# Kernel tuning notes

Measured on AMD Instinct MI355X. Metric: run time of the kernel, lower is better.

Reference implementation:

```python
import jax, jax.numpy as jnp
import numpy as np

N_NODES = 100000
N_EDGES = 1600000
C = 64       # in_channels == filters
K = 3        # Chebyshev order
EPS = 1e-5   # InstanceNorm eps


def setup_inputs() -> dict:
    key = jax.random.key(0)
    ks = jax.random.split(key, 8)
    x = jax.random.normal(ks[0], (N_NODES, C), dtype=jnp.float32)
    edge_index = jax.random.randint(ks[1], (2, N_EDGES), 0, N_NODES, dtype=jnp.int64)
    scale = 1.0 / np.sqrt(C)
    W1 = jax.random.normal(ks[2], (K, C, C), dtype=jnp.float32) * scale
    b1 = jnp.zeros((C,), dtype=jnp.float32)
    W2 = jax.random.normal(ks[3], (K, C, C), dtype=jnp.float32) * scale
    b2 = jnp.zeros((C,), dtype=jnp.float32)
    return {"x": x, "edge_index": edge_index, "W1": W1, "b1": b1, "W2": W2, "b2": b2}


def _cheb_conv(x, src, dst, w_edge, W, b, n):
    # PyG ChebConv, norm='sym', lambda_max=2: L_hat = -D^{-1/2} A D^{-1/2}
    def prop(h):  # h: [N, C] -> L_hat @ h via gather -> weight -> scatter-add
        return jax.ops.segment_sum(w_edge[:, None] * h[src], dst, num_segments=n)
    Tx0 = x
    Tx1 = prop(x)
    Tx2 = 2.0 * prop(Tx1) - Tx0
    return Tx0 @ W[0] + Tx1 @ W[1] + Tx2 @ W[2] + b


def _instance_norm(h):
    # PyG InstanceNorm (single graph, affine=False): normalize over nodes per channel
    m = h.mean(axis=0, keepdims=True)
    v = h.var(axis=0, keepdims=True)
    return (h - m) * jax.lax.rsqrt(v + EPS)


def reference(x, edge_index, W1, b1, W2, b2):
    n = x.shape[0]
    src, dst = edge_index[0], edge_index[1]
    ones = jnp.ones((src.shape[0],), dtype=x.dtype)
    deg = jax.ops.segment_sum(ones, dst, num_segments=n)
    safe = jnp.where(deg > 0, deg, 1.0)
    dinv = jnp.where(deg > 0, jax.lax.rsqrt(safe), 0.0)
    w_edge = -dinv[src] * dinv[dst]  # scaled-Laplacian edge weights
    h = _instance_norm(jax.nn.relu(_cheb_conv(x, src, dst, w_edge, W1, b1, n)))
    h = _instance_norm(jax.nn.relu(_cheb_conv(h, src, dst, w_edge, W2, b2, n)))
    return h
```

## Files before the change

kernel.cpp:

```cpp
#include <hip/hip_runtime.h>
#include <hip/hip_fp16.h>

#define NCH 64
#define EPS 1e-5f
#define SBANKS 32
#define BSHIFT 8
#define NBLKA 256
#define SRCMASK 0x1FFFFu
#define QW_SCALE 32767.0f
#define QW_INV (1.0f/32767.0f)

typedef _Float16 f16x8 __attribute__((ext_vector_type(8)));
typedef float f32x4 __attribute__((ext_vector_type(4)));

__global__ __launch_bounds__(256) void k_front(const float* __restrict__ x, __half* __restrict__ xh,
                                               int castTotal, int castB,
                                               const float* __restrict__ W1, _Float16* __restrict__ Wb1,
                                               const float* __restrict__ W2, _Float16* __restrict__ Wb2,
                                               const int* __restrict__ dst, int* __restrict__ cnt,
                                               int E, int per, int nbuck) {
    int bid = blockIdx.x;
    if (bid < castB) {
        int i = (bid * 256 + threadIdx.x) * 4;
        if (i < castTotal) {
            float4 f = *(const float4*)(x + i);
            __half2* o = (__half2*)(xh + i);
            o[0] = __floats2half2_rn(f.x, f.y);
            o[1] = __floats2half2_rn(f.z, f.w);
        }
        return;
    }
    if (bid < castB + 96) {
        int wb = bid - castB;
        const float* W = (wb < 48) ? W1 : W2;
        _Float16* Wb = (wb < 48) ? Wb1 : Wb2;
        int idx = (wb % 48) * 256 + threadIdx.x;
        int j = idx & 7;
        int lane = (idx >> 3) & 63;
        int tk = idx >> 9;
        int tile = tk / 6, kk = tk % 6;
        int k = kk * 32 + (lane >> 4) * 8 + j;
        int n = tile * 16 + (lane & 15);
        Wb[idx] = (_Float16)W[k * 64 + n];
        return;
    }
    __shared__ int lh[512];
    int hb = bid - castB - 96;
    for (int t = threadIdx.x; t < nbuck; t += 256) lh[t] = 0;
    __syncthreads();
    int lo = hb * per, hi = min(E, lo + per);
    for (int e = lo + threadIdx.x; e < hi; e += 256)
        atomicAdd(&lh[dst[e] >> BSHIFT], 1);
    __syncthreads();
    for (int t = threadIdx.x; t < nbuck; t += 256)
        if (lh[t]) atomicAdd(&cnt[t], lh[t]);
}

__global__ void k_bscan(const int* __restrict__ cnt, int* __restrict__ gbase,
                        int* __restrict__ gcur, int nbuck, int E) {
    __shared__ int s[512];
    int t = threadIdx.x;
    int v = (t < nbuck) ? cnt[t] : 0;
    s[t] = v;
    __syncthreads();
    for (int off = 1; off < 512; off <<= 1) {
        int add = (t >= off) ? s[t - off] : 0;
        __syncthreads();
        s[t] += add;
        __syncthreads();
    }
    if (t < nbuck) { int ex = s[t] - v; gbase[t] = ex; gcur[t] = ex; }
    if (t == 0) gbase[nbuck] = E;
}

__global__ __launch_bounds__(256) void k_bin(const int* __restrict__ src,
                                             const int* __restrict__ dst,
                                             int* __restrict__ gcur,
                                             int2* __restrict__ binned, int E, int per, int nbuck) {
    __shared__ int lh[512];
    __shared__ int lcur[512];
    for (int t = threadIdx.x; t < nbuck; t += 256) lh[t] = 0;
    __syncthreads();
    int lo = blockIdx.x * per, hi = min(E, lo + per);
    for (int e = lo + threadIdx.x; e < hi; e += 256)
        atomicAdd(&lh[dst[e] >> BSHIFT], 1);
    __syncthreads();
    for (int t = threadIdx.x; t < nbuck; t += 256) {
        int c = lh[t];
        lcur[t] = c ? atomicAdd(&gcur[t], c) : 0;
    }
    __syncthreads();
    for (int e = lo + threadIdx.x; e < hi; e += 256) {
        int d = dst[e];
        int b = d >> BSHIFT;
        int pos = atomicAdd(&lcur[b], 1);
        binned[pos] = make_int2(src[e], d);
    }
}

__global__ __launch_bounds__(256) void k_bucket(const int2* __restrict__ binned,
                                                const int* __restrict__ gbase,
                                                float* __restrict__ dinv,
                                                int* __restrict__ rowstart,
                                                unsigned int* __restrict__ csr, int N, int nbuck, int E) {
    __shared__ int hist[256];
    __shared__ int lcur[256];
    __shared__ int ltmp[256];
    int b = blockIdx.x;
    int t = threadIdx.x;
    int nodeLo = b << BSHIFT;
    int nHere = min(256, N - nodeLo);
    int e0 = gbase[b], e1 = gbase[b + 1];
    hist[t] = 0;
    __syncthreads();
    for (int e = e0 + t; e < e1; e += 256)
        atomicAdd(&hist[binned[e].y - nodeLo], 1);
    __syncthreads();
    int deg = (t < nHere) ? hist[t] : 0;
    if (t < nHere) dinv[nodeLo + t] = (deg > 0) ? rsqrtf((float)deg) : 0.0f;
    ltmp[t] = deg;
    __syncthreads();
    for (int off = 1; off < 256; off <<= 1) {
        int add = (t >= off) ? ltmp[t - off] : 0;
        __syncthreads();
        ltmp[t] += add;
        __syncthreads();
    }
    int lstart = ltmp[t] - deg;
    if (t < nHere) rowstart[nodeLo + t] = e0 + lstart;
    if (b == nbuck - 1 && t == 0) rowstart[N] = E;
    lcur[t] = lstart;
    __syncthreads();
    for (int e = e0 + t; e < e1; e += 256) {
        int2 sd = binned[e];
        int dl = sd.y - nodeLo;
        int pos = atomicAdd(&lcur[dl], 1);
        unsigned int dd = (unsigned int)min(hist[dl], 32767);
        csr[e0 + pos] = (unsigned int)sd.x | (dd << 17);
    }
}

__global__ void k_weights(unsigned int* __restrict__ csr, const float* __restrict__ dinv, int E) {
    int e = blockIdx.x * blockDim.x + threadIdx.x;
    if (e < E) {
        unsigned int v = csr[e];
        unsigned int s = v & SRCMASK;
        float dd = rsqrtf((float)(v >> 17));
        float aw = dinv[s] * dd;
        unsigned int qw = (unsigned int)(aw * QW_SCALE + 0.5f);
        csr[e] = s | (qw << 17);
    }
}

__global__ __launch_bounds__(256) void k_prop(const __half* __restrict__ h,
                                              const int* __restrict__ rowstart,
                                              const unsigned int* __restrict__ csr,
                                              const __half* __restrict__ tx0,
                                              __half* __restrict__ y, int N,
                                              const float* __restrict__ gstats,
                                              const float* __restrict__ tstats) {
    int lane = threadIdx.x & 63;
    int wv = (blockIdx.x * 256 + threadIdx.x) >> 6;
    int g = lane >> 3, li = lane & 7;
    int node = wv * 8 + g;
    int e = 0, e1 = 0;
    if (node < N) { e = rowstart[node]; e1 = rowstart[node + 1]; }
    float acc[8] = {0.f, 0.f, 0.f, 0.f, 0.f, 0.f, 0.f, 0.f};
    float sw = 0.0f;
    for (; e + 2 <= e1; e += 2) {
        unsigned int v0 = csr[e], v1 = csr[e + 1];
        uint4 a = *(const uint4*)(h + (size_t)(v0 & SRCMASK) * NCH + li * 8);
        uint4 bq = *(const uint4*)(h + (size_t)(v1 & SRCMASK) * NCH + li * 8);
        float w0 = -(float)(v0 >> 17) * QW_INV;
        float w1 = -(float)(v1 >> 17) * QW_INV;
        sw += w0 + w1;
        float2 f;
        f = __half22float2(*(__half2*)&a.x);  acc[0] = fmaf(w0, f.x, acc[0]); acc[1] = fmaf(w0, f.y, acc[1]);
        f = __half22float2(*(__half2*)&a.y);  acc[2] = fmaf(w0, f.x, acc[2]); acc[3] = fmaf(w0, f.y, acc[3]);
        f = __half22float2(*(__half2*)&a.z);  acc[4] = fmaf(w0, f.x, acc[4]); acc[5] = fmaf(w0, f.y, acc[5]);
        f = __half22float2(*(__half2*)&a.w);  acc[6] = fmaf(w0, f.x, acc[6]); acc[7] = fmaf(w0, f.y, acc[7]);
        f = __half22float2(*(__half2*)&bq.x); acc[0] = fmaf(w1, f.x, acc[0]); acc[1] = fmaf(w1, f.y, acc[1]);
        f = __half22float2(*(__half2*)&bq.y); acc[2] = fmaf(w1, f.x, acc[2]); acc[3] = fmaf(w1, f.y, acc[3]);
        f = __half22float2(*(__half2*)&bq.z); acc[4] = fmaf(w1, f.x, acc[4]); acc[5] = fmaf(w1, f.y, acc[5]);
        f = __half22float2(*(__half2*)&bq.w); acc[6] = fmaf(w1, f.x, acc[6]); acc[7] = fmaf(w1, f.y, acc[7]);
    }
    if (e < e1) {
        unsigned int v0 = csr[e];
        uint4 a = *(const uint4*)(h + (size_t)(v0 & SRCMASK) * NCH + li * 8);
        float w0 = -(float)(v0 >> 17) * QW_INV;
        sw += w0;
        float2 f;
        f = __half22float2(*(__half2*)&a.x);  acc[0] = fmaf(w0, f.x, acc[0]); acc[1] = fmaf(w0, f.y, acc[1]);
        f = __half22float2(*(__half2*)&a.y);  acc[2] = fmaf(w0, f.x, acc[2]); acc[3] = fmaf(w0, f.y, acc[3]);
        f = __half22float2(*(__half2*)&a.z);  acc[4] = fmaf(w0, f.x, acc[4]); acc[5] = fmaf(w0, f.y, acc[5]);
        f = __half22float2(*(__half2*)&a.w);  acc[6] = fmaf(w0, f.x, acc[6]); acc[7] = fmaf(w0, f.y, acc[7]);
    }
    if (node >= N) return;
    if (gstats != nullptr) {
        float4 m0 = *(const float4*)(gstats + li * 8);
        float4 m1 = *(const float4*)(gstats + li * 8 + 4);
        float4 r0 = *(const float4*)(gstats + 64 + li * 8);
        float4 r1 = *(const float4*)(gstats + 64 + li * 8 + 4);
        acc[0] = r0.x * (acc[0] - m0.x * sw);
        acc[1] = r0.y * (acc[1] - m0.y * sw);
        acc[2] = r0.z * (acc[2] - m0.z * sw);
        acc[3] = r0.w * (acc[3] - m0.w * sw);
        acc[4] = r1.x * (acc[4] - m1.x * sw);
        acc[5] = r1.y * (acc[5] - m1.y * sw);
        acc[6] = r1.z * (acc[6] - m1.z * sw);
        acc[7] = r1.w * (acc[7] - m1.w * sw);
    }
    if (tx0 != nullptr) {
        uint4 tq = *(const uint4*)(tx0 + (size_t)node * NCH + li * 8);
        float tv[8];
        float2 f;
        f = __half22float2(*(__half2*)&tq.x); tv[0] = f.x; tv[1] = f.y;
        f = __half22float2(*(__half2*)&tq.y); tv[2] = f.x; tv[3] = f.y;
        f = __half22float2(*(__half2*)&tq.z); tv[4] = f.x; tv[5] = f.y;
        f = __half22float2(*(__half2*)&tq.w); tv[6] = f.x; tv[7] = f.y;
        if (tstats != nullptr) {
            float4 m0 = *(const float4*)(tstats + li * 8);
            float4 m1 = *(const float4*)(tstats + li * 8 + 4);
            float4 r0 = *(const float4*)(tstats + 64 + li * 8);
            float4 r1 = *(const float4*)(tstats + 64 + li * 8 + 4);
            tv[0] = (tv[0] - m0.x) * r0.x; tv[1] = (tv[1] - m0.y) * r0.y;
            tv[2] = (tv[2] - m0.z) * r0.z; tv[3] = (tv[3] - m0.w) * r0.w;
            tv[4] = (tv[4] - m1.x) * r1.x; tv[5] = (tv[5] - m1.y) * r1.y;
            tv[6] = (tv[6] - m1.z) * r1.z; tv[7] = (tv[7] - m1.w) * r1.w;
        }
#pragma unroll
        for (int j = 0; j < 8; j++) acc[j] = 2.0f * acc[j] - tv[j];
    }
    uint4 o;
    __half2 hh;
    hh = __floats2half2_rn(acc[0], acc[1]); o.x = *(unsigned int*)&hh;
    hh = __floats2half2_rn(acc[2], acc[3]); o.y = *(unsigned int*)&hh;
    hh = __floats2half2_rn(acc[4], acc[5]); o.z = *(unsigned int*)&hh;
    hh = __floats2half2_rn(acc[6], acc[7]); o.w = *(unsigned int*)&hh;
    *(uint4*)(y + (size_t)node * NCH + li * 8) = o;
}

template <typename TOUT>
__global__ __launch_bounds__(256) void k_dmm(const __half* __restrict__ tx0,
                                             const __half* __restrict__ tx1,
                                             const __half* __restrict__ tx2,
                                             const _Float16* __restrict__ Wb,
                                             const float* __restrict__ b,
                                             TOUT* __restrict__ out,
                                             float* __restrict__ statsP, int N,
                                             const float* __restrict__ tstats) {
    __shared__ float sred[64];
    __shared__ float sq[64];
    int t = threadIdx.x;
    int w = t >> 6;
    int lane = t & 63;
    if (t < 64) { sred[t] = 0.f; sq[t] = 0.f; }
    __syncthreads();

    int nb16 = blockIdx.x * 64 + w * 16;
    int m = lane & 15, q = lane >> 4;
    int row = nb16 + m;
    int rowC = (row < N) ? row : 0;
    const __half* base0 = tx0 + (size_t)rowC * NCH;
    const __half* base1 = tx1 + (size_t)rowC * NCH;
    const __half* base2 = tx2 + (size_t)rowC * NCH;

    f32x4 acc[4];
#pragma unroll
    for (int tile = 0; tile < 4; tile++) acc[tile] = (f32x4){0.f, 0.f, 0.f, 0.f};

#pragma unroll
    for (int kk = 0; kk < 6; kk++) {
        const __half* ap = (kk < 2 ? base0 : (kk < 4 ? base1 : base2)) + (kk & 1) * 32 + q * 8;
        f16x8 a = *(const f16x8*)ap;
        if (kk < 2 && tstats != nullptr) {
            int cbase = (kk & 1) * 32 + q * 8;
#pragma unroll
            for (int j = 0; j < 8; j++) {
                float v = (float)a[j];
                a[j] = (_Float16)((v - tstats[cbase + j]) * tstats[64 + cbase + j]);
            }
        }
#pragma unroll
        for (int tile = 0; tile < 4; tile++) {
            f16x8 bf = *(const f16x8*)(Wb + ((size_t)(tile * 6 + kk) * 64 + lane) * 8);
            acc[tile] = __builtin_amdgcn_mfma_f32_16x16x32_f16(a, bf, acc[tile], 0, 0, 0);
        }
    }

#pragma unroll
    for (int tile = 0; tile < 4; tile++) {
        int ch = tile * 16 + m;
        float bb = b[ch];
        float s = 0.f, qq = 0.f;
#pragma unroll
        for (int r = 0; r < 4; r++) {
            int node = nb16 + q * 4 + r;
            float v = fmaxf(acc[tile][r] + bb, 0.f);
            if (node < N) {
                out[(size_t)node * NCH + ch] = (TOUT)v;
                s += v;
                qq = fmaf(v, v, qq);
            }
        }
        s += __shfl_xor(s, 16, 64);  s += __shfl_xor(s, 32, 64);
        qq += __shfl_xor(qq, 16, 64); qq += __shfl_xor(qq, 32, 64);
        if (q == 0) { atomicAdd(&sred[ch], s); atomicAdd(&sq[ch], qq); }
    }
    __syncthreads();
    if (t < 64) {
        int bank = blockIdx.x & (SBANKS - 1);
        atomicAdd(&statsP[bank * 128 + t], sred[t]);
        atomicAdd(&statsP[bank * 128 + 64 + t], sq[t]);
    }
}

__global__ void k_final(float* __restrict__ statsP, float invN) {
    int c = threadIdx.x;
    float S = 0.f, Q = 0.f;
    for (int k = 0; k < SBANKS; k++) {
        S += statsP[k * 128 + c];
        Q += statsP[k * 128 + 64 + c];
    }
    float m = S * invN;
    float var = Q * invN - m * m;
    statsP[SBANKS * 128 + c] = m;
    statsP[SBANKS * 128 + 64 + c] = rsqrtf(var + EPS);
}

__global__ void k_norm_f(float* __restrict__ h, const float* __restrict__ statsP, int total) {
    int i = blockIdx.x * blockDim.x + threadIdx.x;
    if (i >= total) return;
    int lane = i & 63;
    h[i] = (h[i] - statsP[SBANKS * 128 + lane]) * statsP[SBANKS * 128 + 64 + lane];
}

extern "C" void kernel_launch(void* const* d_in, const int* in_sizes, int n_in,
                              void* d_out, int out_size, void* d_ws, size_t ws_size,
                              hipStream_t stream) {
    const float* x  = (const float*)d_in[0];
    const int*   ei = (const int*)d_in[1];
    const float* W1 = (const float*)d_in[2];
    const float* b1 = (const float*)d_in[3];
    const float* W2 = (const float*)d_in[4];
    const float* b2 = (const float*)d_in[5];
    float* out = (float*)d_out;

    const int N = in_sizes[0] / NCH;
    const int E = in_sizes[1] / 2;
    const int* src = ei;
    const int* dst = ei + E;
    const int nbuck = (N + 255) >> BSHIFT;

    char* p = (char*)d_ws;
    auto alloc = [&](size_t bytes) {
        void* r = (void*)p;
        p += ((bytes + 255) / 256) * 256;
        return r;
    };
    float*  dinv     = (float*)alloc((size_t)N * 4);
    int*    rowstart = (int*)alloc((size_t)(N + 1) * 4);
    int*    cnt      = (int*)alloc((size_t)nbuck * 4);
    int*    gbase    = (int*)alloc((size_t)(nbuck + 1) * 4);
    int*    gcur     = (int*)alloc((size_t)nbuck * 4);
    unsigned int* csr = (unsigned int*)alloc((size_t)E * 4);
    __half* xh       = (__half*)alloc((size_t)N * NCH * 2);
    __half* Tx1      = (__half*)alloc((size_t)N * NCH * 2);
    __half* Tx2      = (__half*)alloc((size_t)N * NCH * 2);
    __half* A        = (__half*)alloc((size_t)N * NCH * 2);
    _Float16* Wb1    = (_Float16*)alloc(12288 * 2);
    _Float16* Wb2    = (_Float16*)alloc(12288 * 2);
    const int statsFloats = SBANKS * 128 + 128;
    float*  stats    = (float*)alloc((size_t)2 * statsFloats * 4);
    float*  stats1 = stats;
    float*  stats2 = stats + statsFloats;
    const float* nrm1 = stats1 + SBANKS * 128;

    int2* binned = (int2*)Tx1;

    hipMemsetAsync(cnt, 0, (size_t)nbuck * 4, stream);
    hipMemsetAsync(stats, 0, (size_t)2 * statsFloats * 4, stream);

    const int TB = 256;
    const int per = (E + NBLKA - 1) / NBLKA;
    const int castTotal = N * NCH;
    const int castB = (castTotal / 4 + TB - 1) / TB;
    k_front<<<castB + 96 + NBLKA, TB, 0, stream>>>(x, xh, castTotal, castB,
                                                   W1, Wb1, W2, Wb2,
                                                   dst, cnt, E, per, nbuck);
    k_bscan<<<1, 512, 0, stream>>>(cnt, gbase, gcur, nbuck, E);
    k_bin<<<NBLKA, TB, 0, stream>>>(src, dst, gcur, binned, E, per, nbuck);
    k_bucket<<<nbuck, TB, 0, stream>>>(binned, gbase, dinv, rowstart, csr, N, nbuck, E);
    k_weights<<<(E + TB - 1) / TB, TB, 0, stream>>>(csr, dinv, E);

    const int propWaves = (N + 7) / 8;
    const int propBlocks = (propWaves + 3) / 4;
    const int dmmBlocks = (N + 63) / 64;
    const int normBlocks = (N * NCH + TB - 1) / TB;
    const float invN = 1.0f / (float)N;

    k_prop<<<propBlocks, TB, 0, stream>>>(xh, rowstart, csr, nullptr, Tx1, N, nullptr, nullptr);
    k_prop<<<propBlocks, TB, 0, stream>>>(Tx1, rowstart, csr, xh, Tx2, N, nullptr, nullptr);
    k_dmm<__half><<<dmmBlocks, TB, 0, stream>>>(xh, Tx1, Tx2, Wb1, b1, A, stats1, N, nullptr);
    k_final<<<1, 64, 0, stream>>>(stats1, invN);

    k_prop<<<propBlocks, TB, 0, stream>>>(A, rowstart, csr, nullptr, Tx1, N, nrm1, nullptr);
    k_prop<<<propBlocks, TB, 0, stream>>>(Tx1, rowstart, csr, A, Tx2, N, nullptr, nrm1);
    k_dmm<float><<<dmmBlocks, TB, 0, stream>>>(A, Tx1, Tx2, Wb2, b2, out, stats2, N, nrm1);
    k_final<<<1, 64, 0, stream>>>(stats2, invN);
    k_norm_f<<<normBlocks, TB, 0, stream>>>(out, stats2, N * NCH);
}
```

Baseline: 348.8 us.

## Unroll gather loop by four, store layer-2 output in fp16, widen histogram grid

Three separate changes. The gather loop in k_prop now handles four edges per iteration instead of two, putting more loads in flight. The second dense matmul writes fp16 to a scratch buffer, and the final norm kernel reads fp16 and writes fp32 output, which cuts the write-plus-read traffic of the pre-norm tensor. The histogram and binning grid grows from 256 to 1024 blocks. Storing the final pre-norm activations in fp16 adds rounding error to the output.

```diff
diff --git a/kernel.cpp b/kernel.cpp
--- a/kernel.cpp
+++ b/kernel.cpp
@@ -5,7 +5,7 @@
 #define EPS 1e-5f
 #define SBANKS 32
 #define BSHIFT 8
-#define NBLKA 256
+#define NHIST 1024
 #define SRCMASK 0x1FFFFu
 #define QW_SCALE 32767.0f
 #define QW_INV (1.0f/32767.0f)
@@ -152,6 +152,18 @@
     }
 }
 
+__device__ __forceinline__ void edge_acc(const __half* __restrict__ h, unsigned int v,
+                                         int li, float& sw, float (&acc)[8]) {
+    uint4 a = *(const uint4*)(h + (size_t)(v & SRCMASK) * NCH + li * 8);
+    float w = -(float)(v >> 17) * QW_INV;
+    sw += w;
+    float2 f;
+    f = __half22float2(*(__half2*)&a.x); acc[0] = fmaf(w, f.x, acc[0]); acc[1] = fmaf(w, f.y, acc[1]);
+    f = __half22float2(*(__half2*)&a.y); acc[2] = fmaf(w, f.x, acc[2]); acc[3] = fmaf(w, f.y, acc[3]);
+    f = __half22float2(*(__half2*)&a.z); acc[4] = fmaf(w, f.x, acc[4]); acc[5] = fmaf(w, f.y, acc[5]);
+    f = __half22float2(*(__half2*)&a.w); acc[6] = fmaf(w, f.x, acc[6]); acc[7] = fmaf(w, f.y, acc[7]);
+}
+
 __global__ __launch_bounds__(256) void k_prop(const __half* __restrict__ h,
                                               const int* __restrict__ rowstart,
                                               const unsigned int* __restrict__ csr,
@@ -167,33 +179,38 @@
     if (node < N) { e = rowstart[node]; e1 = rowstart[node + 1]; }
     float acc[8] = {0.f, 0.f, 0.f, 0.f, 0.f, 0.f, 0.f, 0.f};
     float sw = 0.0f;
-    for (; e + 2 <= e1; e += 2) {
-        unsigned int v0 = csr[e], v1 = csr[e + 1];
-        uint4 a = *(const uint4*)(h + (size_t)(v0 & SRCMASK) * NCH + li * 8);
-        uint4 bq = *(const uint4*)(h + (size_t)(v1 & SRCMASK) * NCH + li * 8);
+    for (; e + 4 <= e1; e += 4) {
+        unsigned int v0 = csr[e], v1 = csr[e + 1], v2 = csr[e + 2], v3 = csr[e + 3];
+        uint4 a0 = *(const uint4*)(h + (size_t)(v0 & SRCMASK) * NCH + li * 8);
+        uint4 a1 = *(const uint4*)(h + (size_t)(v1 & SRCMASK) * NCH + li * 8);
+        uint4 a2 = *(const uint4*)(h + (size_t)(v2 & SRCMASK) * NCH + li * 8);
+        uint4 a3 = *(const uint4*)(h + (size_t)(v3 & SRCMASK) * NCH + li * 8);
         float w0 = -(float)(v0 >> 17) * QW_INV;
         float w1 = -(float)(v1 >> 17) * QW_INV;
-        sw += w0 + w1;
+        float w2 = -(float)(v2 >> 17) * QW_INV;
+        float w3 = -(float)(v3 >> 17) * QW_INV;
+        sw += (w0 + w1) + (w2 + w3);
         float2 f;
-        f = __half22float2(*(__half2*)&a.x);  acc[0] = fmaf(w0, f.x, acc[0]); acc[1] = fmaf(w0, f.y, acc[1]);
-        f = __half22float2(*(__half2*)&a.y);  acc[2] = fmaf(w0, f.x, acc[2]); acc[3] = fmaf(w0, f.y, acc[3]);
-        f = __half22float2(*(__half2*)&a.z);  acc[4] = fmaf(w0, f.x, acc[4]); acc[5] = fmaf(w0, f.y, acc[5]);
-        f = __half22float2(*(__half2*)&a.w);  acc[6] = fmaf(w0, f.x, acc[6]); acc[7] = fmaf(w0, f.y, acc[7]);
-        f = __half22float2(*(__half2*)&bq.x); acc[0] = fmaf(w1, f.x, acc[0]); acc[1] = fmaf(w1, f.y, acc[1]);
-        f = __half22float2(*(__half2*)&bq.y); acc[2] = fmaf(w1, f.x, acc[2]); acc[3] = fmaf(w1, f.y, acc[3]);
-        f = __half22float2(*(__half2*)&bq.z); acc[4] = fmaf(w1, f.x, acc[4]); acc[5] = fmaf(w1, f.y, acc[5]);
-        f = __half22float2(*(__half2*)&bq.w); acc[6] = fmaf(w1, f.x, acc[6]); acc[7] = fmaf(w1, f.y, acc[7]);
-    }
-    if (e < e1) {
-        unsigned int v0 = csr[e];
-        uint4 a = *(const uint4*)(h + (size_t)(v0 & SRCMASK) * NCH + li * 8);
-        float w0 = -(float)(v0 >> 17) * QW_INV;
-        sw += w0;
-        float2 f;
-        f = __half22float2(*(__half2*)&a.x);  acc[0] = fmaf(w0, f.x, acc[0]); acc[1] = fmaf(w0, f.y, acc[1]);
-        f = __half22float2(*(__half2*)&a.y);  acc[2] = fmaf(w0, f.x, acc[2]); acc[3] = fmaf(w0, f.y, acc[3]);
-        f = __half22float2(*(__half2*)&a.z);  acc[4] = fmaf(w0, f.x, acc[4]); acc[5] = fmaf(w0, f.y, acc[5]);
-        f = __half22float2(*(__half2*)&a.w);  acc[6] = fmaf(w0, f.x, acc[6]); acc[7] = fmaf(w0, f.y, acc[7]);
+        f = __half22float2(*(__half2*)&a0.x); acc[0] = fmaf(w0, f.x, acc[0]); acc[1] = fmaf(w0, f.y, acc[1]);
+        f = __half22float2(*(__half2*)&a0.y); acc[2] = fmaf(w0, f.x, acc[2]); acc[3] = fmaf(w0, f.y, acc[3]);
+        f = __half22float2(*(__half2*)&a0.z); acc[4] = fmaf(w0, f.x, acc[4]); acc[5] = fmaf(w0, f.y, acc[5]);
+        f = __half22float2(*(__half2*)&a0.w); acc[6] = fmaf(w0, f.x, acc[6]); acc[7] = fmaf(w0, f.y, acc[7]);
+        f = __half22float2(*(__half2*)&a1.x); acc[0] = fmaf(w1, f.x, acc[0]); acc[1] = fmaf(w1, f.y, acc[1]);
+        f = __half22float2(*(__half2*)&a1.y); acc[2] = fmaf(w1, f.x, acc[2]); acc[3] = fmaf(w1, f.y, acc[3]);
+        f = __half22float2(*(__half2*)&a1.z); acc[4] = fmaf(w1, f.x, acc[4]); acc[5] = fmaf(w1, f.y, acc[5]);
+        f = __half22float2(*(__half2*)&a1.w); acc[6] = fmaf(w1, f.x, acc[6]); acc[7] = fmaf(w1, f.y, acc[7]);
+        f = __half22float2(*(__half2*)&a2.x); acc[0] = fmaf(w2, f.x, acc[0]); acc[1] = fmaf(w2, f.y, acc[1]);
+        f = __half22float2(*(__half2*)&a2.y); acc[2] = fmaf(w2, f.x, acc[2]); acc[3] = fmaf(w2, f.y, acc[3]);
+        f = __half22float2(*(__half2*)&a2.z); acc[4] = fmaf(w2, f.x, acc[4]); acc[5] = fmaf(w2, f.y, acc[5]);
+        f = __half22float2(*(__half2*)&a2.w); acc[6] = fmaf(w2, f.x, acc[6]); acc[7] = fmaf(w2, f.y, acc[7]);
+        f = __half22float2(*(__half2*)&a3.x); acc[0] = fmaf(w3, f.x, acc[0]); acc[1] = fmaf(w3, f.y, acc[1]);
+        f = __half22float2(*(__half2*)&a3.y); acc[2] = fmaf(w3, f.x, acc[2]); acc[3] = fmaf(w3, f.y, acc[3]);
+        f = __half22float2(*(__half2*)&a3.z); acc[4] = fmaf(w3, f.x, acc[4]); acc[5] = fmaf(w3, f.y, acc[5]);
+        f = __half22float2(*(__half2*)&a3.w); acc[6] = fmaf(w3, f.x, acc[6]); acc[7] = fmaf(w3, f.y, acc[7]);
+    }
+    for (; e < e1; e++) {
+        unsigned int v = csr[e];
+        edge_acc(h, v, li, sw, acc);
     }
     if (node >= N) return;
     if (gstats != nullptr) {
@@ -328,11 +345,12 @@
     statsP[SBANKS * 128 + 64 + c] = rsqrtf(var + EPS);
 }
 
-__global__ void k_norm_f(float* __restrict__ h, const float* __restrict__ statsP, int total) {
+__global__ void k_norm_hf(const __half* __restrict__ a, float* __restrict__ o,
+                          const float* __restrict__ statsP, int total) {
     int i = blockIdx.x * blockDim.x + threadIdx.x;
     if (i >= total) return;
     int lane = i & 63;
-    h[i] = (h[i] - statsP[SBANKS * 128 + lane]) * statsP[SBANKS * 128 + 64 + lane];
+    o[i] = (__half2float(a[i]) - statsP[SBANKS * 128 + lane]) * statsP[SBANKS * 128 + 64 + lane];
 }
 
 extern "C" void kernel_launch(void* const* d_in, const int* in_sizes, int n_in,
@@ -368,6 +386,7 @@
     __half* Tx1      = (__half*)alloc((size_t)N * NCH * 2);
     __half* Tx2      = (__half*)alloc((size_t)N * NCH * 2);
     __half* A        = (__half*)alloc((size_t)N * NCH * 2);
+    __half* A2       = (__half*)alloc((size_t)N * NCH * 2);
     _Float16* Wb1    = (_Float16*)alloc(12288 * 2);
     _Float16* Wb2    = (_Float16*)alloc(12288 * 2);
     const int statsFloats = SBANKS * 128 + 128;
@@ -382,14 +401,14 @@
     hipMemsetAsync(stats, 0, (size_t)2 * statsFloats * 4, stream);
 
     const int TB = 256;
-    const int per = (E + NBLKA - 1) / NBLKA;
+    const int per = (E + NHIST - 1) / NHIST;
     const int castTotal = N * NCH;
     const int castB = (castTotal / 4 + TB - 1) / TB;
-    k_front<<<castB + 96 + NBLKA, TB, 0, stream>>>(x, xh, castTotal, castB,
+    k_front<<<castB + 96 + NHIST, TB, 0, stream>>>(x, xh, castTotal, castB,
                                                    W1, Wb1, W2, Wb2,
                                                    dst, cnt, E, per, nbuck);
     k_bscan<<<1, 512, 0, stream>>>(cnt, gbase, gcur, nbuck, E);
-    k_bin<<<NBLKA, TB, 0, stream>>>(src, dst, gcur, binned, E, per, nbuck);
+    k_bin<<<NHIST, TB, 0, stream>>>(src, dst, gcur, binned, E, per, nbuck);
     k_bucket<<<nbuck, TB, 0, stream>>>(binned, gbase, dinv, rowstart, csr, N, nbuck, E);
     k_weights<<<(E + TB - 1) / TB, TB, 0, stream>>>(csr, dinv, E);
 
@@ -406,7 +425,7 @@
 
     k_prop<<<propBlocks, TB, 0, stream>>>(A, rowstart, csr, nullptr, Tx1, N, nrm1, nullptr);
     k_prop<<<propBlocks, TB, 0, stream>>>(Tx1, rowstart, csr, A, Tx2, N, nullptr, nrm1);
-    k_dmm<float><<<dmmBlocks, TB, 0, stream>>>(A, Tx1, Tx2, Wb2, b2, out, stats2, N, nrm1);
+    k_dmm<__half><<<dmmBlocks, TB, 0, stream>>>(A, Tx1, Tx2, Wb2, b2, A2, stats2, N, nrm1);
     k_final<<<1, 64, 0, stream>>>(stats2, invN);
-    k_norm_f<<<normBlocks, TB, 0, stream>>>(out, stats2, N * NCH);
-}
+    k_norm_hf<<<normBlocks, TB, 0, stream>>>(A2, out, stats2, N * NCH);
+}
```

Result: slower. 362.4 us (+3.9%).
